# Performance work log

Measured on AMD Instinct MI355X. Metric: run time of the kernel, lower is better.

The kernel has to match this reference:

```python
import jax, jax.numpy as jnp
import numpy as np

N, D, L = 8192, 256, 3
DEGREE_P = 0.0078  # ~64 avg degree


def _normalize_adj(g):
    # symmetric normalization with self-loops: D^-1/2 (A + I) D^-1/2
    n = g.shape[0]
    a = g + jnp.eye(n, dtype=g.dtype)
    deg = jnp.sum(a, axis=1)
    dinv = jnp.where(deg > 0, jax.lax.rsqrt(deg), 0.0)
    return a * dinv[:, None] * dinv[None, :]


def _gcn(gn, h, W, b):
    # GCN layer (eval mode, dropout p=0): aggregate -> linear -> relu
    h = gn @ h                      # [N, D] adjacency aggregation
    return jax.nn.relu(h @ W.T + b)  # [N, D]


def setup_inputs() -> dict:
    key = jax.random.key(0)
    ks = jax.random.split(key, 8)
    # sparse binary symmetric adjacency stored dense
    g = (jax.random.uniform(ks[0], (N, N)) < DEGREE_P).astype(jnp.float32)
    g = jnp.maximum(g, g.T)
    h = jax.random.normal(ks[1], (N, D), dtype=jnp.float32)
    s = 1.0 / np.sqrt(D)
    W_down = jax.random.normal(ks[2], (L, D, D), dtype=jnp.float32) * s
    b_down = jnp.zeros((L, D), dtype=jnp.float32)
    W_bottom = jax.random.normal(ks[3], (D, D), dtype=jnp.float32) * s
    b_bottom = jnp.zeros((D,), dtype=jnp.float32)
    W_up = jax.random.normal(ks[4], (L, D, D), dtype=jnp.float32) * s
    b_up = jnp.zeros((L, D), dtype=jnp.float32)
    return dict(g=g, h=h, W_down=W_down, b_down=b_down,
                W_bottom=W_bottom, b_bottom=b_bottom,
                W_up=W_up, b_up=b_up)


def reference(g, h, W_down, b_down, W_bottom, b_bottom, W_up, b_up):
    gn = _normalize_adj(g)
    l_n = W_down.shape[0]
    org_h = h
    down_outs = []
    for i in range(l_n):
        h = _gcn(gn, h, W_down[i], b_down[i])
        down_outs.append(h)
    h = _gcn(gn, h, W_bottom, b_bottom)
    hs = []
    for i in range(l_n):
        h = h + down_outs[l_n - i - 1]   # skip connection
        h = _gcn(gn, h, W_up[i], b_up[i])
        hs.append(h)
    hs.append(h + org_h)
    return jnp.stack(hs)  # [l_n+1, N, D]
```

## Files before the change

### kernel.cpp

```cpp
#include <hip/hip_runtime.h>
#include <cstdint>
#include <cstddef>


#define GN 8192
#define GD 256
#define CAP 320

typedef unsigned int uint32;
using frag_ab = __attribute__((ext_vector_type(8))) short;
using frag_cd = __attribute__((ext_vector_type(4))) float;

static __device__ inline unsigned short f2bf(float x) {
    uint32 u = __float_as_uint(x);
    u += 0x7fffu + ((u >> 16) & 1u);
    return (unsigned short)(u >> 16);
}

__global__ __launch_bounds__(256) void k_build(const float* __restrict__ g,
                                               unsigned short* __restrict__ col,
                                               int* __restrict__ cnt,
                                               float* __restrict__ dinv)
{
    __shared__ int s_cnt;
    const int i = blockIdx.x;
    const int tid = threadIdx.x;
    if (tid == 0) s_cnt = 0;
    __syncthreads();
    const float4* grow = (const float4*)(g + (size_t)i * GN);
    unsigned short* crow = col + (size_t)i * CAP;
    for (int j4 = tid; j4 < GN / 4; j4 += 256) {
        float4 v = grow[j4];
        int j = j4 * 4;
        if (v.x != 0.0f) { int p = atomicAdd(&s_cnt, 1); if (p < CAP) crow[p] = (unsigned short)(j + 0); }
        if (v.y != 0.0f) { int p = atomicAdd(&s_cnt, 1); if (p < CAP) crow[p] = (unsigned short)(j + 1); }
        if (v.z != 0.0f) { int p = atomicAdd(&s_cnt, 1); if (p < CAP) crow[p] = (unsigned short)(j + 2); }
        if (v.w != 0.0f) { int p = atomicAdd(&s_cnt, 1); if (p < CAP) crow[p] = (unsigned short)(j + 3); }
    }
    __syncthreads();
    if (tid == 0) {
        int n = s_cnt; if (n > CAP) n = CAP;
        cnt[i] = n;
        dinv[i] = rsqrtf((float)s_cnt + 1.0f);
    }
}

__global__ __launch_bounds__(256) void k_scale(const float* __restrict__ h,
                                               const float* __restrict__ dinv,
                                               unsigned short* __restrict__ hs_bf)
{
    int idx = blockIdx.x * 256 + threadIdx.x;
    float4 v = ((const float4*)h)[idx];
    int row = idx / (GD / 4);
    float dv = dinv[row];
    ushort4 r;
    r.x = f2bf(v.x * dv); r.y = f2bf(v.y * dv);
    r.z = f2bf(v.z * dv); r.w = f2bf(v.w * dv);
    ((ushort4*)hs_bf)[idx] = r;
}

__global__ __launch_bounds__(256) void k_f2bf(const float* __restrict__ src,
                                              unsigned short* __restrict__ dst)
{
    int idx = blockIdx.x * 256 + threadIdx.x;
    float4 v = ((const float4*)src)[idx];
    ushort4 r;
    r.x = f2bf(v.x); r.y = f2bf(v.y); r.z = f2bf(v.z); r.w = f2bf(v.w);
    ((ushort4*)dst)[idx] = r;
}

__global__ __launch_bounds__(256) void k_spmm(const uint32* __restrict__ hsw,
                                              const unsigned short* __restrict__ col,
                                              const int* __restrict__ cnt,
                                              const float* __restrict__ dinv,
                                              uint32* __restrict__ yw)
{
    __shared__ unsigned short s_cols[4][CAP];
    const int tid = threadIdx.x;
    const int lr = tid >> 6;
    const int lane = tid & 63;
    const int i = blockIdx.x * 4 + lr;
    const int base = blockIdx.y * 64 + lane;
    const int n = cnt[i];
    unsigned short* sc = s_cols[lr];
    for (int t = lane; t < n; t += 64) sc[t] = col[(size_t)i * CAP + t];

    float alo = 0.f, ahi = 0.f;
    int t = 0;
    for (; t + 4 <= n; t += 4) {
        int c0 = sc[t], c1 = sc[t + 1], c2 = sc[t + 2], c3 = sc[t + 3];
        uint32 u0 = hsw[(size_t)c0 * 128 + base];
        uint32 u1 = hsw[(size_t)c1 * 128 + base];
        uint32 u2 = hsw[(size_t)c2 * 128 + base];
        uint32 u3 = hsw[(size_t)c3 * 128 + base];
        alo += __uint_as_float(u0 << 16); ahi += __uint_as_float(u0 & 0xffff0000u);
        alo += __uint_as_float(u1 << 16); ahi += __uint_as_float(u1 & 0xffff0000u);
        alo += __uint_as_float(u2 << 16); ahi += __uint_as_float(u2 & 0xffff0000u);
        alo += __uint_as_float(u3 << 16); ahi += __uint_as_float(u3 & 0xffff0000u);
    }
    for (; t < n; ++t) {
        uint32 u = hsw[(size_t)sc[t] * 128 + base];
        alo += __uint_as_float(u << 16); ahi += __uint_as_float(u & 0xffff0000u);
    }
    uint32 us = hsw[(size_t)i * 128 + base];
    alo += __uint_as_float(us << 16); ahi += __uint_as_float(us & 0xffff0000u);
    float dv = dinv[i];
    alo *= dv; ahi *= dv;
    yw[(size_t)i * 128 + base] = (uint32)f2bf(alo) | ((uint32)f2bf(ahi) << 16);
}

__global__ __launch_bounds__(256) void k_gemm(const unsigned short* __restrict__ Y,
                                              const unsigned short* __restrict__ W,
                                              const float* __restrict__ bias,
                                              const float* __restrict__ dinv,
                                              const float* __restrict__ skip,
                                              float* __restrict__ h_out,
                                              unsigned short* __restrict__ hs_out,
                                              float* __restrict__ sum_out,
                                              const float* __restrict__ add_src)
{
    const int tid  = threadIdx.x;
    const int w    = tid >> 6;
    const int lane = tid & 63;
    const int quad = lane >> 4;
    const int l16  = lane & 15;
    const int m0 = blockIdx.x * 64 + w * 16;
    const int n0 = blockIdx.y * 64;

    frag_cd acc0 = {0.f,0.f,0.f,0.f}, acc1 = {0.f,0.f,0.f,0.f};
    frag_cd acc2 = {0.f,0.f,0.f,0.f}, acc3 = {0.f,0.f,0.f,0.f};

    const size_t abase  = (size_t)(m0 + l16) * GD + quad * 8;
    const size_t bbase0 = (size_t)(n0 +  0 + l16) * GD + quad * 8;
    const size_t bbase1 = (size_t)(n0 + 16 + l16) * GD + quad * 8;
    const size_t bbase2 = (size_t)(n0 + 32 + l16) * GD + quad * 8;
    const size_t bbase3 = (size_t)(n0 + 48 + l16) * GD + quad * 8;

#pragma unroll
    for (int k0 = 0; k0 < GD; k0 += 32) {
        frag_ab a  = *(const frag_ab*)(Y + abase  + k0);
        frag_ab b0 = *(const frag_ab*)(W + bbase0 + k0);
        frag_ab b1 = *(const frag_ab*)(W + bbase1 + k0);
        frag_ab b2 = *(const frag_ab*)(W + bbase2 + k0);
        frag_ab b3 = *(const frag_ab*)(W + bbase3 + k0);
        acc0 = __builtin_amdgcn_mfma_f32_16x16x32_bf16(a, b0, acc0, 0, 0, 0);
        acc1 = __builtin_amdgcn_mfma_f32_16x16x32_bf16(a, b1, acc1, 0, 0, 0);
        acc2 = __builtin_amdgcn_mfma_f32_16x16x32_bf16(a, b2, acc2, 0, 0, 0);
        acc3 = __builtin_amdgcn_mfma_f32_16x16x32_bf16(a, b3, acc3, 0, 0, 0);
    }

    const float bn0 = bias[n0 +  0 + l16];
    const float bn1 = bias[n0 + 16 + l16];
    const float bn2 = bias[n0 + 32 + l16];
    const float bn3 = bias[n0 + 48 + l16];

#pragma unroll
    for (int reg = 0; reg < 4; ++reg) {
        const int m = m0 + quad * 4 + reg;
        const float dv = dinv[m];
        const size_t rbase = (size_t)m * GD + l16;
        float v[4];
        v[0] = fmaxf(acc0[reg] + bn0, 0.f);
        v[1] = fmaxf(acc1[reg] + bn1, 0.f);
        v[2] = fmaxf(acc2[reg] + bn2, 0.f);
        v[3] = fmaxf(acc3[reg] + bn3, 0.f);
#pragma unroll
        for (int nt = 0; nt < 4; ++nt) {
            const size_t idx = rbase + n0 * 0 + nt * 16 + n0;
        }
#pragma unroll
        for (int nt = 0; nt < 4; ++nt) {
            const size_t idx = (size_t)m * GD + n0 + nt * 16 + l16;
            const float x = v[nt];
            if (h_out)  h_out[idx] = x;
            if (hs_out) {
                float s = skip ? skip[idx] : 0.f;
                hs_out[idx] = f2bf(dv * (x + s));
            }
            if (sum_out) sum_out[idx] = x + add_src[idx];
        }
    }
}

extern "C" void kernel_launch(void* const* d_in, const int* in_sizes, int n_in,
                              void* d_out, int out_size, void* d_ws, size_t ws_size,
                              hipStream_t stream)
{
    const float* g  = (const float*)d_in[0];
    const float* h  = (const float*)d_in[1];
    const float* Wd = (const float*)d_in[2];
    const float* bd = (const float*)d_in[3];
    const float* Wb = (const float*)d_in[4];
    const float* bb = (const float*)d_in[5];
    const float* Wu = (const float*)d_in[6];
    const float* bu = (const float*)d_in[7];
    float* out = (float*)d_out;

    char* ws = (char*)d_ws;
    float*          dinv = (float*)ws;
    int*            cnt  = (int*)(ws + 32 * 1024);
    unsigned short* col  = (unsigned short*)(ws + 64 * 1024);
    size_t off = 64 * 1024 + (size_t)GN * CAP * sizeof(unsigned short);
    off = (off + 255) & ~(size_t)255;
    unsigned short* hs_bf = (unsigned short*)(ws + off); off += (size_t)GN * GD * 2;
    unsigned short* y_bf  = (unsigned short*)(ws + off); off += (size_t)GN * GD * 2;
    unsigned short* w_bf  = (unsigned short*)(ws + off); off += (size_t)7 * GD * GD * 2;
    off = (off + 255) & ~(size_t)255;
    float* dbuf1 = (float*)(ws + off); off += (size_t)GN * GD * 4;
    float* dbuf2 = (float*)(ws + off); off += (size_t)GN * GD * 4;
    float* dbuf3 = (float*)(ws + off); off += (size_t)GN * GD * 4;
    (void)ws_size; (void)in_sizes; (void)n_in; (void)out_size;

    const size_t ND = (size_t)GN * GD;
    const int WSZ = GD * GD;
    dim3 ggrid(GN / 64, GD / 64);
    dim3 sgrid(GN / 4, 2);

    k_build<<<GN, 256, 0, stream>>>(g, col, cnt, dinv);
    k_scale<<<GN * GD / 4 / 256, 256, 0, stream>>>(h, dinv, hs_bf);
    k_f2bf<<<3 * WSZ / 4 / 256, 256, 0, stream>>>(Wd, w_bf + 0 * (size_t)WSZ);
    k_f2bf<<<1 * WSZ / 4 / 256, 256, 0, stream>>>(Wb, w_bf + 3 * (size_t)WSZ);
    k_f2bf<<<3 * WSZ / 4 / 256, 256, 0, stream>>>(Wu, w_bf + 4 * (size_t)WSZ);

    k_spmm<<<sgrid, 256, 0, stream>>>((const uint32*)hs_bf, col, cnt, dinv, (uint32*)y_bf);
    k_gemm<<<ggrid, 256, 0, stream>>>(y_bf, w_bf + 0 * (size_t)WSZ, bd + 0 * GD, dinv, nullptr, dbuf1, hs_bf, nullptr, nullptr);
    k_spmm<<<sgrid, 256, 0, stream>>>((const uint32*)hs_bf, col, cnt, dinv, (uint32*)y_bf);
    k_gemm<<<ggrid, 256, 0, stream>>>(y_bf, w_bf + 1 * (size_t)WSZ, bd + 1 * GD, dinv, nullptr, dbuf2, hs_bf, nullptr, nullptr);
    k_spmm<<<sgrid, 256, 0, stream>>>((const uint32*)hs_bf, col, cnt, dinv, (uint32*)y_bf);
    k_gemm<<<ggrid, 256, 0, stream>>>(y_bf, w_bf + 2 * (size_t)WSZ, bd + 2 * GD, dinv, nullptr, dbuf3, hs_bf, nullptr, nullptr);

    k_spmm<<<sgrid, 256, 0, stream>>>((const uint32*)hs_bf, col, cnt, dinv, (uint32*)y_bf);
    k_gemm<<<ggrid, 256, 0, stream>>>(y_bf, w_bf + 3 * (size_t)WSZ, bb, dinv, dbuf3, nullptr, hs_bf, nullptr, nullptr);

    k_spmm<<<sgrid, 256, 0, stream>>>((const uint32*)hs_bf, col, cnt, dinv, (uint32*)y_bf);
    k_gemm<<<ggrid, 256, 0, stream>>>(y_bf, w_bf + 4 * (size_t)WSZ, bu + 0 * GD, dinv, dbuf2, out + 0 * ND, hs_bf, nullptr, nullptr);
    k_spmm<<<sgrid, 256, 0, stream>>>((const uint32*)hs_bf, col, cnt, dinv, (uint32*)y_bf);
    k_gemm<<<ggrid, 256, 0, stream>>>(y_bf, w_bf + 5 * (size_t)WSZ, bu + 1 * GD, dinv, dbuf1, out + 1 * ND, hs_bf, nullptr, nullptr);
    k_spmm<<<sgrid, 256, 0, stream>>>((const uint32*)hs_bf, col, cnt, dinv, (uint32*)y_bf);
    k_gemm<<<ggrid, 256, 0, stream>>>(y_bf, w_bf + 6 * (size_t)WSZ, bu + 2 * GD, dinv, nullptr, out + 2 * ND, nullptr, out + 3 * ND, h);
}
```

Before: 699.1 us.

## Split SpMM neighbor loop across lane groups with shuffle reduction

The SpMM kernel now has each wave's four 16-lane groups cover a 16-column slice and split the neighbor list between them, then combine partial sums with cross-lane shuffles. The grid becomes 8 column blocks by N/4 row blocks. Neighbor lists are padded to a multiple of four with the row's own index, and the self-loop weight is corrected to account for the padding. The aim is more independent loads in flight per row and less serialization over long neighbor lists. The cost is narrower 64-byte row segments per gather and extra shuffle work.

Result: slower. 811.8 us (+16.1%).

```diff
diff --git a/kernel.cpp b/kernel.cpp
--- a/kernel.cpp
+++ b/kernel.cpp
@@ -42,6 +42,9 @@
         int n = s_cnt; if (n > CAP) n = CAP;
         cnt[i] = n;
         dinv[i] = rsqrtf((float)s_cnt + 1.0f);
+        int pad = (4 - (n & 3)) & 3;
+        for (int k = 0; k < pad; ++k)
+            if (n + k < CAP) crow[n + k] = (unsigned short)i;
     }
 }
 
@@ -76,37 +79,57 @@
                                               uint32* __restrict__ yw)
 {
     __shared__ unsigned short s_cols[4][CAP];
-    const int tid = threadIdx.x;
-    const int lr = tid >> 6;
+    const int tid  = threadIdx.x;
+    const int lr   = tid >> 6;
     const int lane = tid & 63;
-    const int i = blockIdx.x * 4 + lr;
-    const int base = blockIdx.y * 64 + lane;
-    const int n = cnt[i];
+    const int j    = lane >> 4;
+    const int q    = lane & 15;
+    const int i     = blockIdx.y * 4 + lr;
+    const int cbase = blockIdx.x * 16 + q;
+    const int n  = cnt[i];
+    const int n4 = (n + 3) & ~3;
     unsigned short* sc = s_cols[lr];
-    for (int t = lane; t < n; t += 64) sc[t] = col[(size_t)i * CAP + t];
+    for (int t = lane; t < n4; t += 64) sc[t] = col[(size_t)i * CAP + t];
 
     float alo = 0.f, ahi = 0.f;
-    int t = 0;
-    for (; t + 4 <= n; t += 4) {
-        int c0 = sc[t], c1 = sc[t + 1], c2 = sc[t + 2], c3 = sc[t + 3];
-        uint32 u0 = hsw[(size_t)c0 * 128 + base];
-        uint32 u1 = hsw[(size_t)c1 * 128 + base];
-        uint32 u2 = hsw[(size_t)c2 * 128 + base];
-        uint32 u3 = hsw[(size_t)c3 * 128 + base];
+    int t = j;
+    for (; t + 28 < n4; t += 32) {
+        int c0 = sc[t], c1 = sc[t + 4], c2 = sc[t + 8],  c3 = sc[t + 12];
+        int c4 = sc[t + 16], c5 = sc[t + 20], c6 = sc[t + 24], c7 = sc[t + 28];
+        uint32 u0 = hsw[(size_t)c0 * 128 + cbase];
+        uint32 u1 = hsw[(size_t)c1 * 128 + cbase];
+        uint32 u2 = hsw[(size_t)c2 * 128 + cbase];
+        uint32 u3 = hsw[(size_t)c3 * 128 + cbase];
+        uint32 u4 = hsw[(size_t)c4 * 128 + cbase];
+        uint32 u5 = hsw[(size_t)c5 * 128 + cbase];
+        uint32 u6 = hsw[(size_t)c6 * 128 + cbase];
+        uint32 u7 = hsw[(size_t)c7 * 128 + cbase];
         alo += __uint_as_float(u0 << 16); ahi += __uint_as_float(u0 & 0xffff0000u);
         alo += __uint_as_float(u1 << 16); ahi += __uint_as_float(u1 & 0xffff0000u);
         alo += __uint_as_float(u2 << 16); ahi += __uint_as_float(u2 & 0xffff0000u);
         alo += __uint_as_float(u3 << 16); ahi += __uint_as_float(u3 & 0xffff0000u);
-    }
-    for (; t < n; ++t) {
-        uint32 u = hsw[(size_t)sc[t] * 128 + base];
+        alo += __uint_as_float(u4 << 16); ahi += __uint_as_float(u4 & 0xffff0000u);
+        alo += __uint_as_float(u5 << 16); ahi += __uint_as_float(u5 & 0xffff0000u);
+        alo += __uint_as_float(u6 << 16); ahi += __uint_as_float(u6 & 0xffff0000u);
+        alo += __uint_as_float(u7 << 16); ahi += __uint_as_float(u7 & 0xffff0000u);
+    }
+    for (; t < n4; t += 4) {
+        uint32 u = hsw[(size_t)sc[t] * 128 + cbase];
         alo += __uint_as_float(u << 16); ahi += __uint_as_float(u & 0xffff0000u);
     }
-    uint32 us = hsw[(size_t)i * 128 + base];
-    alo += __uint_as_float(us << 16); ahi += __uint_as_float(us & 0xffff0000u);
-    float dv = dinv[i];
-    alo *= dv; ahi *= dv;
-    yw[(size_t)i * 128 + base] = (uint32)f2bf(alo) | ((uint32)f2bf(ahi) << 16);
+
+    alo += __shfl_xor(alo, 16, 64); ahi += __shfl_xor(ahi, 16, 64);
+    alo += __shfl_xor(alo, 32, 64); ahi += __shfl_xor(ahi, 32, 64);
+
+    if (j == 0) {
+        uint32 us = hsw[(size_t)i * 128 + cbase];
+        float slo = __uint_as_float(us << 16);
+        float shi = __uint_as_float(us & 0xffff0000u);
+        float coeff = (float)(1 - (n4 - n));
+        alo += coeff * slo; ahi += coeff * shi;
+        float dv = dinv[i];
+        yw[(size_t)i * 128 + cbase] = (uint32)f2bf(alo * dv) | ((uint32)f2bf(ahi * dv) << 16);
+    }
 }
 
 __global__ __launch_bounds__(256) void k_gemm(const unsigned short* __restrict__ Y,
@@ -158,16 +181,11 @@
     for (int reg = 0; reg < 4; ++reg) {
         const int m = m0 + quad * 4 + reg;
         const float dv = dinv[m];
-        const size_t rbase = (size_t)m * GD + l16;
         float v[4];
         v[0] = fmaxf(acc0[reg] + bn0, 0.f);
         v[1] = fmaxf(acc1[reg] + bn1, 0.f);
         v[2] = fmaxf(acc2[reg] + bn2, 0.f);
         v[3] = fmaxf(acc3[reg] + bn3, 0.f);
-#pragma unroll
-        for (int nt = 0; nt < 4; ++nt) {
-            const size_t idx = rbase + n0 * 0 + nt * 16 + n0;
-        }
 #pragma unroll
         for (int nt = 0; nt < 4; ++nt) {
             const size_t idx = (size_t)m * GD + n0 + nt * 16 + l16;
@@ -214,7 +232,7 @@
     const size_t ND = (size_t)GN * GD;
     const int WSZ = GD * GD;
     dim3 ggrid(GN / 64, GD / 64);
-    dim3 sgrid(GN / 4, 2);
+    dim3 sgrid(8, GN / 4);
 
     k_build<<<GN, 256, 0, stream>>>(g, col, cnt, dinv);
     k_scale<<<GN * GD / 4 / 256, 256, 0, stream>>>(h, dinv, hs_bf);
```

## Restructure SpMM gather: one wave per row, 8-byte loads, padded scalar indices

Applied to the files above, without the earlier changes.

The SpMM kernel now has one wavefront cover a full 256-wide row, and each lane loads 8 bytes (four bf16 values) instead of 4. This halves the grid and drops the second column block. Neighbor indices are read as packed uint4 groups and broadcast with readfirstlane instead of being staged through shared memory. The build kernel pads each column list to a multiple of 8 with the row's own index, and the self-loop term is scaled to cancel the padding. This removes the tail loop and the LDS staging, at the cost of a few redundant gathers of the row itself per row.

Result: slower. 785.3 us (+12.3%).

```diff
diff --git a/kernel.cpp b/kernel.cpp
--- a/kernel.cpp
+++ b/kernel.cpp
@@ -42,6 +42,9 @@
         int n = s_cnt; if (n > CAP) n = CAP;
         cnt[i] = n;
         dinv[i] = rsqrtf((float)s_cnt + 1.0f);
+        int n8 = (n + 7) & ~7;
+        for (int k = n; k < n8; ++k)
+            if (k < CAP) crow[k] = (unsigned short)i;
     }
 }
 
@@ -75,38 +78,68 @@
                                               const float* __restrict__ dinv,
                                               uint32* __restrict__ yw)
 {
-    __shared__ unsigned short s_cols[4][CAP];
-    const int tid = threadIdx.x;
-    const int lr = tid >> 6;
+    const int tid  = threadIdx.x;
+    const int lw   = tid >> 6;
     const int lane = tid & 63;
-    const int i = blockIdx.x * 4 + lr;
-    const int base = blockIdx.y * 64 + lane;
+    const int i = blockIdx.x * 4 + lw;
     const int n = cnt[i];
-    unsigned short* sc = s_cols[lr];
-    for (int t = lane; t < n; t += 64) sc[t] = col[(size_t)i * CAP + t];
-
-    float alo = 0.f, ahi = 0.f;
-    int t = 0;
-    for (; t + 4 <= n; t += 4) {
-        int c0 = sc[t], c1 = sc[t + 1], c2 = sc[t + 2], c3 = sc[t + 3];
-        uint32 u0 = hsw[(size_t)c0 * 128 + base];
-        uint32 u1 = hsw[(size_t)c1 * 128 + base];
-        uint32 u2 = hsw[(size_t)c2 * 128 + base];
-        uint32 u3 = hsw[(size_t)c3 * 128 + base];
-        alo += __uint_as_float(u0 << 16); ahi += __uint_as_float(u0 & 0xffff0000u);
-        alo += __uint_as_float(u1 << 16); ahi += __uint_as_float(u1 & 0xffff0000u);
-        alo += __uint_as_float(u2 << 16); ahi += __uint_as_float(u2 & 0xffff0000u);
-        alo += __uint_as_float(u3 << 16); ahi += __uint_as_float(u3 & 0xffff0000u);
-    }
-    for (; t < n; ++t) {
-        uint32 u = hsw[(size_t)sc[t] * 128 + base];
-        alo += __uint_as_float(u << 16); ahi += __uint_as_float(u & 0xffff0000u);
-    }
-    uint32 us = hsw[(size_t)i * 128 + base];
-    alo += __uint_as_float(us << 16); ahi += __uint_as_float(us & 0xffff0000u);
-    float dv = dinv[i];
-    alo *= dv; ahi *= dv;
-    yw[(size_t)i * 128 + base] = (uint32)f2bf(alo) | ((uint32)f2bf(ahi) << 16);
+    int n8 = (n + 7) & ~7; if (n8 > CAP) n8 = CAP;
+    const uint4* idxp = (const uint4*)(col + (size_t)i * CAP);
+    const uint32* lbase = hsw + lane * 2;
+
+    float a0=0.f,a1=0.f,a2=0.f,a3=0.f;
+    float b0=0.f,b1=0.f,b2=0.f,b3=0.f;
+
+    for (int t8 = 0; t8 < n8; t8 += 8) {
+        uint4 packed = idxp[t8 >> 3];
+        uint32 p0 = (uint32)__builtin_amdgcn_readfirstlane((int)packed.x);
+        uint32 p1 = (uint32)__builtin_amdgcn_readfirstlane((int)packed.y);
+        uint32 p2 = (uint32)__builtin_amdgcn_readfirstlane((int)packed.z);
+        uint32 p3 = (uint32)__builtin_amdgcn_readfirstlane((int)packed.w);
+        const int c0 = (int)(p0 & 0xffffu), c1 = (int)(p0 >> 16);
+        const int c2 = (int)(p1 & 0xffffu), c3 = (int)(p1 >> 16);
+        const int c4 = (int)(p2 & 0xffffu), c5 = (int)(p2 >> 16);
+        const int c6 = (int)(p3 & 0xffffu), c7 = (int)(p3 >> 16);
+        uint2 u0 = *(const uint2*)(lbase + (size_t)c0 * 128);
+        uint2 u1 = *(const uint2*)(lbase + (size_t)c1 * 128);
+        uint2 u2 = *(const uint2*)(lbase + (size_t)c2 * 128);
+        uint2 u3 = *(const uint2*)(lbase + (size_t)c3 * 128);
+        uint2 u4 = *(const uint2*)(lbase + (size_t)c4 * 128);
+        uint2 u5 = *(const uint2*)(lbase + (size_t)c5 * 128);
+        uint2 u6 = *(const uint2*)(lbase + (size_t)c6 * 128);
+        uint2 u7 = *(const uint2*)(lbase + (size_t)c7 * 128);
+        a0 += __uint_as_float(u0.x << 16); a1 += __uint_as_float(u0.x & 0xffff0000u);
+        a2 += __uint_as_float(u0.y << 16); a3 += __uint_as_float(u0.y & 0xffff0000u);
+        b0 += __uint_as_float(u1.x << 16); b1 += __uint_as_float(u1.x & 0xffff0000u);
+        b2 += __uint_as_float(u1.y << 16); b3 += __uint_as_float(u1.y & 0xffff0000u);
+        a0 += __uint_as_float(u2.x << 16); a1 += __uint_as_float(u2.x & 0xffff0000u);
+        a2 += __uint_as_float(u2.y << 16); a3 += __uint_as_float(u2.y & 0xffff0000u);
+        b0 += __uint_as_float(u3.x << 16); b1 += __uint_as_float(u3.x & 0xffff0000u);
+        b2 += __uint_as_float(u3.y << 16); b3 += __uint_as_float(u3.y & 0xffff0000u);
+        a0 += __uint_as_float(u4.x << 16); a1 += __uint_as_float(u4.x & 0xffff0000u);
+        a2 += __uint_as_float(u4.y << 16); a3 += __uint_as_float(u4.y & 0xffff0000u);
+        b0 += __uint_as_float(u5.x << 16); b1 += __uint_as_float(u5.x & 0xffff0000u);
+        b2 += __uint_as_float(u5.y << 16); b3 += __uint_as_float(u5.y & 0xffff0000u);
+        a0 += __uint_as_float(u6.x << 16); a1 += __uint_as_float(u6.x & 0xffff0000u);
+        a2 += __uint_as_float(u6.y << 16); a3 += __uint_as_float(u6.y & 0xffff0000u);
+        b0 += __uint_as_float(u7.x << 16); b1 += __uint_as_float(u7.x & 0xffff0000u);
+        b2 += __uint_as_float(u7.y << 16); b3 += __uint_as_float(u7.y & 0xffff0000u);
+    }
+
+    uint2 us = *(const uint2*)(lbase + (size_t)i * 128);
+    const float coeff = (float)(1 - (n8 - n));
+    a0 += coeff * __uint_as_float(us.x << 16);
+    a1 += coeff * __uint_as_float(us.x & 0xffff0000u);
+    a2 += coeff * __uint_as_float(us.y << 16);
+    a3 += coeff * __uint_as_float(us.y & 0xffff0000u);
+
+    const float dv = dinv[i];
+    a0 = (a0 + b0) * dv; a1 = (a1 + b1) * dv;
+    a2 = (a2 + b2) * dv; a3 = (a3 + b3) * dv;
+    uint2 r;
+    r.x = (uint32)f2bf(a0) | ((uint32)f2bf(a1) << 16);
+    r.y = (uint32)f2bf(a2) | ((uint32)f2bf(a3) << 16);
+    *(uint2*)(yw + (size_t)i * 128 + lane * 2) = r;
 }
 
 __global__ __launch_bounds__(256) void k_gemm(const unsigned short* __restrict__ Y,
@@ -158,16 +191,11 @@
     for (int reg = 0; reg < 4; ++reg) {
         const int m = m0 + quad * 4 + reg;
         const float dv = dinv[m];
-        const size_t rbase = (size_t)m * GD + l16;
         float v[4];
         v[0] = fmaxf(acc0[reg] + bn0, 0.f);
         v[1] = fmaxf(acc1[reg] + bn1, 0.f);
         v[2] = fmaxf(acc2[reg] + bn2, 0.f);
         v[3] = fmaxf(acc3[reg] + bn3, 0.f);
-#pragma unroll
-        for (int nt = 0; nt < 4; ++nt) {
-            const size_t idx = rbase + n0 * 0 + nt * 16 + n0;
-        }
 #pragma unroll
         for (int nt = 0; nt < 4; ++nt) {
             const size_t idx = (size_t)m * GD + n0 + nt * 16 + l16;
@@ -214,7 +242,7 @@
     const size_t ND = (size_t)GN * GD;
     const int WSZ = GD * GD;
     dim3 ggrid(GN / 64, GD / 64);
-    dim3 sgrid(GN / 4, 2);
+    dim3 sgrid(GN / 4);
 
     k_build<<<GN, 256, 0, stream>>>(g, col, cnt, dinv);
     k_scale<<<GN * GD / 4 / 256, 256, 0, stream>>>(h, dinv, hs_bf);
```
